# Performance work log

Hardware: AMD Instinct MI355X
Metric: run time of the kernel (lower is better)

The kernel has to match this reference:

```python
import jax, jax.numpy as jnp
import numpy as np

B, D, H, O, E = 8192, 1024, 4096, 1024, 3

def setup_inputs() -> dict:
    key = jax.random.key(0)
    ks = jax.random.split(key, 8)
    s = lambda fan_in: 1.0 / np.sqrt(fan_in)
    return {
        "x":   jax.random.normal(ks[0], (B, D), jnp.float32),
        "gw1": jax.random.normal(ks[1], (D, 256), jnp.float32) * s(D),
        "gb1": jnp.zeros((256,), jnp.float32),
        "gw2": jax.random.normal(ks[2], (256, 128), jnp.float32) * s(256),
        "gb2": jnp.zeros((128,), jnp.float32),
        "gw3": jax.random.normal(ks[3], (128, E), jnp.float32) * s(128),
        "gb3": jnp.zeros((E,), jnp.float32),
        "ew1": jax.random.normal(ks[4], (E, D, H), jnp.float32) * s(D),
        "eb1": jnp.zeros((E, H), jnp.float32),
        "ew2": jax.random.normal(ks[5], (E, H, O), jnp.float32) * s(H),
        "eb2": jnp.zeros((E, O), jnp.float32),
        "top_k": 2,
    }

def reference(x, gw1, gb1, gw2, gb2, gw3, gb3, ew1, eb1, ew2, eb2, top_k):
    # Gating network (dropout is identity in eval mode)
    g = jax.nn.relu(x @ gw1 + gb1)
    g = jax.nn.relu(g @ gw2 + gb2)
    gates = jax.nn.softmax(g @ gw3 + gb3, axis=-1)          # [B, E]

    # top-k routing with renormalized weights
    topk_scores, topk_idx = jax.lax.top_k(gates, top_k)     # [B, k]
    topk_scores = topk_scores / jnp.sum(topk_scores, axis=-1, keepdims=True)

    # scatter normalized scores into dense [B, E] combine weights
    b_ix = jnp.arange(x.shape[0])[:, None]
    combine = jnp.zeros_like(gates).at[b_ix, topk_idx].add(topk_scores)  # [B, E]

    # run all experts densely (small E=3), combine with routing weights
    eh = jax.nn.relu(jnp.einsum('bd,edh->beh', x, ew1) + eb1[None])      # [B, E, H]
    eo = jnp.einsum('beh,eho->beo', eh, ew2) + eb2[None]                 # [B, E, O]
    out = jnp.einsum('be,beo->bo', combine, eo)                          # [B, O]
    return out, gates
```

## Files before the change

### kernel.cpp

```cpp
#include <hip/hip_runtime.h>
#include <cstdint>
#include <cstddef>

#define B_ROWS 8192
#define D_DIM  1024
#define H_DIM  4096
#define O_DIM  1024
#define E_NUM  3
#define K2     (2 * H_DIM)
#define MT256  34
#define SLOT_MAX (MT256 * 256)

typedef __attribute__((ext_vector_type(4))) float f4;
typedef __attribute__((ext_vector_type(8))) _Float16 half8;

__device__ __forceinline__ unsigned short f2h_bits(float f) {
  _Float16 h = (_Float16)f;
  return __builtin_bit_cast(unsigned short, h);
}

__device__ __forceinline__ void async16(const void* g, void* l) {
  __builtin_amdgcn_global_load_lds(
      (const __attribute__((address_space(1))) unsigned int*)g,
      (__attribute__((address_space(3))) unsigned int*)l, 16, 0, 0);
}

__global__ __launch_bounds__(256) void k_cast_x(const float* __restrict__ in,
                                                unsigned short* __restrict__ out) {
  size_t i = (size_t)blockIdx.x * 256 + threadIdx.x;
  const f4* p = (const f4*)in;
  f4 a = p[2 * i], b = p[2 * i + 1];
  half8 h;
#pragma unroll
  for (int j = 0; j < 4; ++j) { h[j] = (_Float16)a[j]; h[4 + j] = (_Float16)b[j]; }
  *(half8*)(out + 8 * i) = h;
}

__global__ __launch_bounds__(256) void k_transpose_cast(const float* __restrict__ in,
                                                        unsigned short* __restrict__ out,
                                                        int R, int C) {
  __shared__ float tile[32][33];
  const size_t eoff = (size_t)blockIdx.z * R * C;
  const float* I = in + eoff;
  unsigned short* O = out + eoff;
  int c0 = blockIdx.x * 32, r0 = blockIdx.y * 32;
  int tx = threadIdx.x & 31, ty = threadIdx.x >> 5;
#pragma unroll
  for (int i = 0; i < 4; ++i)
    tile[ty + 8 * i][tx] = I[(size_t)(r0 + ty + 8 * i) * C + c0 + tx];
  __syncthreads();
#pragma unroll
  for (int i = 0; i < 4; ++i)
    O[(size_t)(c0 + ty + 8 * i) * R + r0 + tx] = f2h_bits(tile[tx][ty + 8 * i]);
}

__global__ __launch_bounds__(256) void k_gemm_f32(const float* __restrict__ A,
                                                  const float* __restrict__ Bm,
                                                  const float* __restrict__ bias,
                                                  float* __restrict__ C,
                                                  int N, int K) {
  __shared__ float sAT[16][68];
  __shared__ float sB[16][68];
  const int t = threadIdx.x;
  const int tx = t & 15, ty = t >> 4;
  const int m0 = blockIdx.y * 64, n0 = blockIdx.x * 64;
  float acc[4][4] = {};
  for (int k0 = 0; k0 < K; k0 += 16) {
    __syncthreads();
#pragma unroll
    for (int i = 0; i < 4; ++i) {
      int idx = t + i * 256;
      int r = idx >> 4, c = idx & 15;
      sAT[c][r] = A[(size_t)(m0 + r) * K + (k0 + c)];
      int rb = idx >> 6, cb = idx & 63;
      sB[rb][cb] = Bm[(size_t)(k0 + rb) * N + (n0 + cb)];
    }
    __syncthreads();
#pragma unroll
    for (int kk = 0; kk < 16; ++kk) {
      f4 av = *(const f4*)&sAT[kk][ty * 4];
      f4 bv = *(const f4*)&sB[kk][tx * 4];
#pragma unroll
      for (int i = 0; i < 4; ++i)
#pragma unroll
        for (int j = 0; j < 4; ++j)
          acc[i][j] = fmaf(av[i], bv[j], acc[i][j]);
    }
  }
#pragma unroll
  for (int i = 0; i < 4; ++i) {
    int row = m0 + ty * 4 + i;
    f4 v;
#pragma unroll
    for (int j = 0; j < 4; ++j)
      v[j] = fmaxf(acc[i][j] + bias[n0 + tx * 4 + j], 0.f);
    *(f4*)&C[(size_t)row * N + n0 + tx * 4] = v;
  }
}

__global__ __launch_bounds__(256) void k_gate_topk(const float* __restrict__ h2,
                                                   const float* __restrict__ gw3,
                                                   const float* __restrict__ gb3,
                                                   float* __restrict__ gates,
                                                   float* __restrict__ combine,
                                                   int* __restrict__ bucket) {
  const int lane = threadIdx.x & 63;
  const int row = blockIdx.x * 4 + (threadIdx.x >> 6);
  const float* h = h2 + (size_t)row * 128;
  float h0 = h[lane], h1 = h[lane + 64];
  float l0 = h0 * gw3[lane * 3 + 0] + h1 * gw3[(lane + 64) * 3 + 0];
  float l1 = h0 * gw3[lane * 3 + 1] + h1 * gw3[(lane + 64) * 3 + 1];
  float l2 = h0 * gw3[lane * 3 + 2] + h1 * gw3[(lane + 64) * 3 + 2];
#pragma unroll
  for (int off = 32; off > 0; off >>= 1) {
    l0 += __shfl_down(l0, off);
    l1 += __shfl_down(l1, off);
    l2 += __shfl_down(l2, off);
  }
  if (lane == 0) {
    float g0 = l0 + gb3[0], g1v = l1 + gb3[1], g2v = l2 + gb3[2];
    float mx = fmaxf(g0, fmaxf(g1v, g2v));
    float e0 = expf(g0 - mx), e1 = expf(g1v - mx), e2 = expf(g2v - mx);
    float inv = 1.f / (e0 + e1 + e2);
    float p0 = e0 * inv, p1 = e1 * inv, p2 = e2 * inv;
    gates[row * 3 + 0] = p0; gates[row * 3 + 1] = p1; gates[row * 3 + 2] = p2;
    int amin = 0; float pm = p0;
    if (p1 <= pm) { pm = p1; amin = 1; }
    if (p2 <= pm) { pm = p2; amin = 2; }
    float denom = (p0 + p1 + p2) - pm;
    combine[row * 3 + 0] = (amin == 0) ? 0.f : p0 / denom;
    combine[row * 3 + 1] = (amin == 1) ? 0.f : p1 / denom;
    combine[row * 3 + 2] = (amin == 2) ? 0.f : p2 / denom;
    bucket[row] = amin;
  }
}

__global__ __launch_bounds__(256) void k_count(const int* __restrict__ bucket,
                                               int* __restrict__ cnt) {
  int row = blockIdx.x * 256 + threadIdx.x;
  int b = bucket[row];
  int lane = threadIdx.x & 63;
#pragma unroll
  for (int bid = 0; bid < 3; ++bid) {
    unsigned long long m = __ballot(b == bid);
    if (m && b == bid) {
      int prefix = __popcll(m & ((1ull << lane) - 1));
      if (prefix == 0) atomicAdd(&cnt[bid], __popcll(m));
    }
  }
}

__global__ void k_meta(const int* __restrict__ cnt, int* __restrict__ meta,
                       int* __restrict__ cnt2) {
  int t0 = (cnt[0] + 255) >> 8;
  int t1 = (cnt[1] + 255) >> 8;
  int t2 = (cnt[2] + 255) >> 8;
  meta[0] = 0; meta[1] = t0; meta[2] = t0 + t1; meta[3] = t0 + t1 + t2;
  cnt2[0] = 0; cnt2[1] = 0; cnt2[2] = 0;
}

__global__ __launch_bounds__(256) void k_scatter(const int* __restrict__ bucket,
                                                 const int* __restrict__ meta,
                                                 int* __restrict__ cnt2,
                                                 int* __restrict__ sorted) {
  int row = blockIdx.x * 256 + threadIdx.x;
  int b = bucket[row];
  int lane = threadIdx.x & 63;
#pragma unroll
  for (int bid = 0; bid < 3; ++bid) {
    unsigned long long m = __ballot(b == bid);
    if (m) {
      int cntm = __popcll(m);
      int leader = __ffsll((unsigned long long)m) - 1;
      int base = 0;
      if (lane == leader) base = atomicAdd(&cnt2[bid], cntm);
      base = __shfl(base, leader);
      if (b == bid) {
        int prefix = __popcll(m & ((1ull << lane) - 1));
        sorted[meta[bid] * 256 + base + prefix] = row;
      }
    }
  }
}

__device__ __forceinline__ void bucket_experts(int b, int& ea, int& eb) {
  ea = (b == 0) ? 1 : 0;
  eb = (b == 2) ? 1 : 2;
}


#define BAR8()  do { __builtin_amdgcn_s_barrier(); __builtin_amdgcn_sched_barrier(0); } while (0)
#define LGKM0() do { asm volatile("s_waitcnt lgkmcnt(0)" ::: "memory"); __builtin_amdgcn_sched_barrier(0); } while (0)
#define VMW(n)  do { asm volatile("s_waitcnt vmcnt(" #n ")" ::: "memory"); __builtin_amdgcn_sched_barrier(0); } while (0)

#define STG_A(buf, h, kt) do { \
    async16(aptr[(h) * 2 + 0] + (size_t)(kt) * 64, smem + (buf) * 32768 + (h) * 16384 + t * 16); \
    async16(aptr[(h) * 2 + 1] + (size_t)(kt) * 64, smem + (buf) * 32768 + (h) * 16384 + 8192 + t * 16); \
  } while (0)
#define STG_B(buf, h, kt) do { \
    async16(bptr[(h) * 2 + 0] + (size_t)(kt) * 64, smem + 65536 + (buf) * 32768 + (h) * 16384 + t * 16); \
    async16(bptr[(h) * 2 + 1] + (size_t)(kt) * 64, smem + 65536 + (buf) * 32768 + (h) * 16384 + 8192 + t * 16); \
  } while (0)
#define LDA8(buf, mh) do { \
    _Pragma("unroll") \
    for (int mf = 0; mf < 4; ++mf) { \
      fa[mf][0] = *(const half8*)(smem + (buf) * 32768 + baseA + (mh) * 8192 + mf * 2048 + ck0); \
      fa[mf][1] = *(const half8*)(smem + (buf) * 32768 + baseA + (mh) * 8192 + mf * 2048 + ck1); \
    } } while (0)
#define LDB8(buf, nh) do { \
    _Pragma("unroll") \
    for (int nf2 = 0; nf2 < 2; ++nf2) { \
      fb[(nh) * 2 + nf2][0] = *(const half8*)(smem + (buf) * 32768 + baseB + ((nh) * 2 + nf2) * 2048 + ck0); \
      fb[(nh) * 2 + nf2][1] = *(const half8*)(smem + (buf) * 32768 + baseB + ((nh) * 2 + nf2) * 2048 + ck1); \
    } } while (0)
#define MM8(mh, nh) do { \
    _Pragma("unroll") \
    for (int mf = 0; mf < 4; ++mf) { \
      _Pragma("unroll") \
      for (int nf2 = 0; nf2 < 2; ++nf2) { \
        acc[(mh) * 4 + mf][(nh) * 2 + nf2] = __builtin_amdgcn_mfma_f32_16x16x32_f16( \
            fa[mf][0], fb[(nh) * 2 + nf2][0], acc[(mh) * 4 + mf][(nh) * 2 + nf2], 0, 0, 0); \
        acc[(mh) * 4 + mf][(nh) * 2 + nf2] = __builtin_amdgcn_mfma_f32_16x16x32_f16( \
            fa[mf][1], fb[(nh) * 2 + nf2][1], acc[(mh) * 4 + mf][(nh) * 2 + nf2], 0, 0, 0); \
      } } } while (0)

__global__ __launch_bounds__(512, 2) void k_expert_h8(const unsigned short* __restrict__ Xh,
                                                      const unsigned short* __restrict__ W1T,
                                                      const float* __restrict__ combine,
                                                      const float* __restrict__ eb1,
                                                      const int* __restrict__ sorted,
                                                      const int* __restrict__ meta,
                                                      unsigned short* __restrict__ EHS) {
  constexpr int K = D_DIM;
  const int mt = blockIdx.x;
  const int tb1 = meta[1], tb2 = meta[2], tb3 = meta[3];
  if (mt >= tb3) return;
  const int b = (mt >= tb2) ? 2 : (mt >= tb1) ? 1 : 0;
  int ea, ebx; bucket_experts(b, ea, ebx);
  const int z = blockIdx.z;
  const int e = z ? ebx : ea;
  const int slot0 = mt * 256;
  const int n0 = blockIdx.y * 256;

  __shared__ __align__(16) char smem[131072];
  __shared__ float sC[256];
  const int t = threadIdx.x;
  if (t < 256) {
    int r = sorted[slot0 + t];
    sC[t] = (r < 0) ? 0.f : combine[(size_t)r * 3 + e];
  }

  const int jrow = t >> 3;
  const int j = (t & 7) ^ (jrow & 7);
  const unsigned short* aptr[4];
  const unsigned short* bptr[4];
#pragma unroll
  for (int i = 0; i < 4; ++i) {
    int R = jrow + i * 64;
    int r = sorted[slot0 + R];
    int rr = (r < 0) ? 0 : r;
    aptr[i] = Xh + (size_t)rr * K + j * 8;
    bptr[i] = W1T + (size_t)e * H_DIM * K + (size_t)(n0 + R) * K + j * 8;
  }
  const int lane = t & 63;
  const int wid = t >> 6;
  const int wm = wid >> 2, wn = wid & 3;
  const int quad = lane >> 4, l16 = lane & 15;
  const int ck0 = ((quad) ^ (l16 & 7)) * 16;
  const int ck1 = ((4 + quad) ^ (l16 & 7)) * 16;
  const int baseA = (wm * 128 + l16) * 128;
  const int baseB = 65536 + (wn * 64 + l16) * 128;

  f4 acc[8][4] = {};
  half8 fa[4][2], fb[4][2];

  STG_A(0, 0, 0); STG_A(0, 1, 0); STG_B(0, 0, 0); STG_B(0, 1, 0);
  STG_B(1, 0, 1); STG_B(1, 1, 1);
  VMW(4); BAR8();

#pragma unroll 1
  for (int it = 0; it < 7; ++it) {
    const int kt = 2 * it;
    LDA8(0, 0); LDB8(0, 0); STG_A(1, 0, kt + 1);
    BAR8(); LGKM0();
    __builtin_amdgcn_s_setprio(1); MM8(0, 0); __builtin_amdgcn_s_setprio(0);
    BAR8();
    LDB8(0, 1); STG_A(1, 1, kt + 1);
    BAR8(); LGKM0();
    __builtin_amdgcn_s_setprio(1); MM8(0, 1); __builtin_amdgcn_s_setprio(0);
    BAR8();
    LDA8(0, 1); STG_B(0, 0, kt + 2);
    BAR8(); LGKM0();
    __builtin_amdgcn_s_setprio(1); MM8(1, 0); __builtin_amdgcn_s_setprio(0);
    BAR8();
    STG_A(0, 0, kt + 2);
    BAR8(); LGKM0();
    __builtin_amdgcn_s_setprio(1); MM8(1, 1); __builtin_amdgcn_s_setprio(0);
    VMW(4); BAR8();
    LDA8(1, 0); LDB8(1, 0); STG_A(0, 1, kt + 2);
    BAR8(); LGKM0();
    __builtin_amdgcn_s_setprio(1); MM8(0, 0); __builtin_amdgcn_s_setprio(0);
    BAR8();
    LDB8(1, 1); STG_B(0, 1, kt + 2);
    BAR8(); LGKM0();
    __builtin_amdgcn_s_setprio(1); MM8(0, 1); __builtin_amdgcn_s_setprio(0);
    BAR8();
    LDA8(1, 1); STG_B(1, 0, kt + 3);
    BAR8(); LGKM0();
    __builtin_amdgcn_s_setprio(1); MM8(1, 0); __builtin_amdgcn_s_setprio(0);
    BAR8();
    STG_B(1, 1, kt + 3);
    BAR8(); LGKM0();
    __builtin_amdgcn_s_setprio(1); MM8(1, 1); __builtin_amdgcn_s_setprio(0);
    VMW(4); BAR8();
  }
  {
    LDA8(0, 0); LDB8(0, 0); STG_A(1, 0, 15);
    BAR8(); LGKM0();
    __builtin_amdgcn_s_setprio(1); MM8(0, 0); __builtin_amdgcn_s_setprio(0);
    BAR8();
    LDB8(0, 1); STG_A(1, 1, 15);
    BAR8(); LGKM0();
    __builtin_amdgcn_s_setprio(1); MM8(0, 1); __builtin_amdgcn_s_setprio(0);
    BAR8();
    LDA8(0, 1);
    BAR8(); LGKM0();
    __builtin_amdgcn_s_setprio(1); MM8(1, 0); __builtin_amdgcn_s_setprio(0);
    BAR8();
    BAR8(); LGKM0();
    __builtin_amdgcn_s_setprio(1); MM8(1, 1); __builtin_amdgcn_s_setprio(0);
    VMW(0); BAR8();
    LDA8(1, 0); LDB8(1, 0); MM8(0, 0);
    LDB8(1, 1); MM8(0, 1);
    LDA8(1, 1); MM8(1, 0);
    MM8(1, 1);
  }

  const float* bias = eb1 + (size_t)e * H_DIM;
#pragma unroll
  for (int nf = 0; nf < 4; ++nf) {
    int col = n0 + wn * 64 + nf * 16 + l16;
    float bb = bias[col];
#pragma unroll
    for (int mf = 0; mf < 8; ++mf) {
#pragma unroll
      for (int r = 0; r < 4; ++r) {
        int rloc = wm * 128 + mf * 16 + quad * 4 + r;
        float v = fmaxf(acc[mf][nf][r] + bb, 0.f) * sC[rloc];
        EHS[(size_t)(slot0 + rloc) * K2 + (size_t)z * H_DIM + col] = f2h_bits(v);
      }
    }
  }
}

__global__ __launch_bounds__(256) void k_expert_o(const unsigned short* __restrict__ EHS,
                                                  const unsigned short* __restrict__ W2T,
                                                  const float* __restrict__ combine,
                                                  const float* __restrict__ eb2,
                                                  const int* __restrict__ sorted,
                                                  const int* __restrict__ meta,
                                                  float* __restrict__ OUT) {
  const int mt = blockIdx.x;
  const int tb1 = meta[1] * 2, tb2 = meta[2] * 2, tb3 = meta[3] * 2;
  if (mt >= tb3) return;
  const int b = (mt >= tb2) ? 2 : (mt >= tb1) ? 1 : 0;
  int ea, ebx; bucket_experts(b, ea, ebx);
  const int hz = blockIdx.z;
  const int e = hz ? ebx : ea;
  const int slot0 = mt * 128;
  const int n0 = blockIdx.y * 128;

  __shared__ __align__(16) char smem[32768];
  __shared__ int sRow[128];
  __shared__ float sCa[128], sCb[128];
  char* sA = smem;
  char* sB = smem + 16384;
  const int t = threadIdx.x;
  if (t < 128) {
    int r = sorted[slot0 + t];
    sRow[t] = r;
    int rr = (r < 0) ? 0 : r;
    sCa[t] = combine[(size_t)rr * 3 + ea];
    sCb[t] = combine[(size_t)rr * 3 + ebx];
  }

  const unsigned short* ap[4];
  size_t bpo[4];
  int soff[4];
#pragma unroll
  for (int i = 0; i < 4; ++i) {
    int sa = t + i * 256;
    int row = sa >> 3;
    int j = (sa & 7) ^ (row & 7);
    soff[i] = sa * 16;
    ap[i] = EHS + (size_t)(slot0 + row) * K2 + (size_t)hz * H_DIM + j * 8;
    bpo[i] = (size_t)(n0 + row) * H_DIM + j * 8;
  }
  const int lane = t & 63;
  const int wm = (t >> 6) & 1, wn = t >> 7;
  const int quad = lane >> 4, l16 = lane & 15;
  int offA[4][2], offB[4][2];
#pragma unroll
  for (int mtile = 0; mtile < 4; ++mtile) {
    int ra = wm * 64 + mtile * 16 + l16;
    int rb = wn * 64 + mtile * 16 + l16;
#pragma unroll
    for (int s = 0; s < 2; ++s) {
      offA[mtile][s] = ra * 128 + (((s * 4 + quad) ^ (ra & 7)) * 16);
      offB[mtile][s] = rb * 128 + (((s * 4 + quad) ^ (rb & 7)) * 16);
    }
  }
  f4 acc[4][4] = {};
  const unsigned short* Bb = W2T + (size_t)e * O_DIM * H_DIM;
  for (int k0 = 0; k0 < H_DIM; k0 += 64) {
#pragma unroll
    for (int i = 0; i < 4; ++i) {
      async16(ap[i] + k0, sA + soff[i]);
      async16(Bb + bpo[i] + k0, sB + soff[i]);
    }
    __syncthreads();
#pragma unroll
    for (int s = 0; s < 2; ++s) {
      half8 a[4], bfr[4];
#pragma unroll
      for (int i = 0; i < 4; ++i) a[i] = *(const half8*)(sA + offA[i][s]);
#pragma unroll
      for (int i = 0; i < 4; ++i) bfr[i] = *(const half8*)(sB + offB[i][s]);
#pragma unroll
      for (int i = 0; i < 4; ++i)
#pragma unroll
        for (int jn = 0; jn < 4; ++jn)
          acc[i][jn] = __builtin_amdgcn_mfma_f32_16x16x32_f16(a[i], bfr[jn], acc[i][jn], 0, 0, 0);
    }
    __syncthreads();
  }
#pragma unroll
  for (int nt = 0; nt < 4; ++nt) {
    int col = n0 + wn * 64 + nt * 16 + l16;
    float ba = eb2[(size_t)ea * O_DIM + col];
    float bb = eb2[(size_t)ebx * O_DIM + col];
#pragma unroll
    for (int mtile = 0; mtile < 4; ++mtile) {
#pragma unroll
      for (int r = 0; r < 4; ++r) {
        int rloc = wm * 64 + mtile * 16 + quad * 4 + r;
        int rowg = sRow[rloc];
        if (rowg >= 0) {
          float v = acc[mtile][nt][r];
          if (hz == 0) v += sCa[rloc] * ba + sCb[rloc] * bb;
          atomicAdd(&OUT[(size_t)rowg * O_DIM + col], v);
        }
      }
    }
  }
}

extern "C" void kernel_launch(void* const* d_in, const int* in_sizes, int n_in,
                              void* d_out, int out_size, void* d_ws, size_t ws_size,
                              hipStream_t stream) {
  const float* x   = (const float*)d_in[0];
  const float* gw1 = (const float*)d_in[1];
  const float* gb1 = (const float*)d_in[2];
  const float* gw2 = (const float*)d_in[3];
  const float* gb2 = (const float*)d_in[4];
  const float* gw3 = (const float*)d_in[5];
  const float* gb3 = (const float*)d_in[6];
  const float* ew1 = (const float*)d_in[7];
  const float* eb1 = (const float*)d_in[8];
  const float* ew2 = (const float*)d_in[9];
  const float* eb2 = (const float*)d_in[10];
  float* out = (float*)d_out;
  float* gates = out + (size_t)B_ROWS * O_DIM;

  char* ws = (char*)d_ws;
  size_t off = 0;
  auto take = [&](size_t bytes) -> char* {
    char* p = ws + off;
    off += (bytes + 255) & ~(size_t)255;
    return p;
  };
  unsigned short* xh  = (unsigned short*)take((size_t)B_ROWS * D_DIM * 2);
  unsigned short* w1t = (unsigned short*)take((size_t)E_NUM * H_DIM * D_DIM * 2);
  unsigned short* w2t = (unsigned short*)take((size_t)E_NUM * O_DIM * H_DIM * 2);
  float* comb   = (float*)take((size_t)B_ROWS * 3 * 4);
  float* g1     = (float*)take((size_t)B_ROWS * 256 * 4);
  float* h2     = (float*)take((size_t)B_ROWS * 128 * 4);
  int* bucket   = (int*)take((size_t)B_ROWS * 4);
  int* sorted   = (int*)take((size_t)SLOT_MAX * 4);
  int* cnt      = (int*)take(3 * 4);
  int* cnt2     = (int*)take(3 * 4);
  int* meta     = (int*)take(4 * 4);
  unsigned short* ehs = (unsigned short*)take((size_t)SLOT_MAX * K2 * 2);

  hipMemsetAsync(cnt, 0, 3 * 4, stream);
  hipMemsetAsync(sorted, 0xFF, (size_t)SLOT_MAX * 4, stream);
  hipMemsetAsync(out, 0, (size_t)B_ROWS * O_DIM * 4, stream);

  k_cast_x<<<dim3(B_ROWS * D_DIM / (256 * 8)), 256, 0, stream>>>(x, xh);
  k_transpose_cast<<<dim3(H_DIM / 32, D_DIM / 32, E_NUM), 256, 0, stream>>>(ew1, w1t, D_DIM, H_DIM);
  k_transpose_cast<<<dim3(O_DIM / 32, H_DIM / 32, E_NUM), 256, 0, stream>>>(ew2, w2t, H_DIM, O_DIM);

  k_gemm_f32<<<dim3(256 / 64, B_ROWS / 64), 256, 0, stream>>>(x, gw1, gb1, g1, 256, D_DIM);
  k_gemm_f32<<<dim3(128 / 64, B_ROWS / 64), 256, 0, stream>>>(g1, gw2, gb2, h2, 128, 256);
  k_gate_topk<<<dim3(B_ROWS / 4), 256, 0, stream>>>(h2, gw3, gb3, gates, comb, bucket);

  k_count<<<dim3(B_ROWS / 256), 256, 0, stream>>>(bucket, cnt);
  k_meta<<<1, 1, 0, stream>>>(cnt, meta, cnt2);
  k_scatter<<<dim3(B_ROWS / 256), 256, 0, stream>>>(bucket, meta, cnt2, sorted);

  k_expert_h8<<<dim3(MT256, H_DIM / 256, 2), 512, 0, stream>>>(
      xh, w1t, comb, eb1, sorted, meta, ehs);
  k_expert_o<<<dim3(MT256 * 2, O_DIM / 128, 2), 256, 0, stream>>>(
      ehs, w2t, comb, eb2, sorted, meta, out);
}
```

Baseline: 846.1 us.

## Port second expert GEMM to 256x256 pipelined 8-wave MFMA kernel

Factors the software-pipelined K loop of the first expert GEMM into a macro and reuses it for the second expert GEMM. The second GEMM moves from 128x128 tiles with 256 threads and a simple load-sync-compute loop to 256x256 tiles with 512 threads, double-buffered async LDS staging and interleaved MFMA phases. The aim is more data reuse per tile and better overlap of global loads with matrix math over the long K=4096 reduction. In exchange the grid has a quarter as many blocks, which can underfill the GPU, and each block needs a large LDS allocation and more registers. There is also a leftover unused per-row load of sorted indices.

```diff
diff --git a/kernel.cpp b/kernel.cpp
--- a/kernel.cpp
+++ b/kernel.cpp
@@ -224,6 +224,65 @@
             fa[mf][1], fb[(nh) * 2 + nf2][1], acc[(mh) * 4 + mf][(nh) * 2 + nf2], 0, 0, 0); \
       } } } while (0)
 
+#define KLOOP8(NITER, LASTKT) \
+  _Pragma("unroll 1") \
+  for (int it = 0; it < (NITER) - 1; ++it) { \
+    const int kt = 2 * it; \
+    LDA8(0, 0); LDB8(0, 0); STG_A(1, 0, kt + 1); \
+    BAR8(); LGKM0(); \
+    __builtin_amdgcn_s_setprio(1); MM8(0, 0); __builtin_amdgcn_s_setprio(0); \
+    BAR8(); \
+    LDB8(0, 1); STG_A(1, 1, kt + 1); \
+    BAR8(); LGKM0(); \
+    __builtin_amdgcn_s_setprio(1); MM8(0, 1); __builtin_amdgcn_s_setprio(0); \
+    BAR8(); \
+    LDA8(0, 1); STG_B(0, 0, kt + 2); \
+    BAR8(); LGKM0(); \
+    __builtin_amdgcn_s_setprio(1); MM8(1, 0); __builtin_amdgcn_s_setprio(0); \
+    BAR8(); \
+    STG_A(0, 0, kt + 2); \
+    BAR8(); LGKM0(); \
+    __builtin_amdgcn_s_setprio(1); MM8(1, 1); __builtin_amdgcn_s_setprio(0); \
+    VMW(4); BAR8(); \
+    LDA8(1, 0); LDB8(1, 0); STG_A(0, 1, kt + 2); \
+    BAR8(); LGKM0(); \
+    __builtin_amdgcn_s_setprio(1); MM8(0, 0); __builtin_amdgcn_s_setprio(0); \
+    BAR8(); \
+    LDB8(1, 1); STG_B(0, 1, kt + 2); \
+    BAR8(); LGKM0(); \
+    __builtin_amdgcn_s_setprio(1); MM8(0, 1); __builtin_amdgcn_s_setprio(0); \
+    BAR8(); \
+    LDA8(1, 1); STG_B(1, 0, kt + 3); \
+    BAR8(); LGKM0(); \
+    __builtin_amdgcn_s_setprio(1); MM8(1, 0); __builtin_amdgcn_s_setprio(0); \
+    BAR8(); \
+    STG_B(1, 1, kt + 3); \
+    BAR8(); LGKM0(); \
+    __builtin_amdgcn_s_setprio(1); MM8(1, 1); __builtin_amdgcn_s_setprio(0); \
+    VMW(4); BAR8(); \
+  } \
+  {  \
+    LDA8(0, 0); LDB8(0, 0); STG_A(1, 0, LASTKT); \
+    BAR8(); LGKM0(); \
+    __builtin_amdgcn_s_setprio(1); MM8(0, 0); __builtin_amdgcn_s_setprio(0); \
+    BAR8(); \
+    LDB8(0, 1); STG_A(1, 1, LASTKT); \
+    BAR8(); LGKM0(); \
+    __builtin_amdgcn_s_setprio(1); MM8(0, 1); __builtin_amdgcn_s_setprio(0); \
+    BAR8(); \
+    LDA8(0, 1); \
+    BAR8(); LGKM0(); \
+    __builtin_amdgcn_s_setprio(1); MM8(1, 0); __builtin_amdgcn_s_setprio(0); \
+    BAR8(); \
+    BAR8(); LGKM0(); \
+    __builtin_amdgcn_s_setprio(1); MM8(1, 1); __builtin_amdgcn_s_setprio(0); \
+    VMW(0); BAR8(); \
+    LDA8(1, 0); LDB8(1, 0); MM8(0, 0); \
+    LDB8(1, 1); MM8(0, 1); \
+    LDA8(1, 1); MM8(1, 0); \
+    MM8(1, 1); \
+  }
+
 __global__ __launch_bounds__(512, 2) void k_expert_h8(const unsigned short* __restrict__ Xh,
                                                       const unsigned short* __restrict__ W1T,
                                                       const float* __restrict__ combine,
@@ -278,63 +337,7 @@
   STG_B(1, 0, 1); STG_B(1, 1, 1);
   VMW(4); BAR8();
 
-#pragma unroll 1
-  for (int it = 0; it < 7; ++it) {
-    const int kt = 2 * it;
-    LDA8(0, 0); LDB8(0, 0); STG_A(1, 0, kt + 1);
-    BAR8(); LGKM0();
-    __builtin_amdgcn_s_setprio(1); MM8(0, 0); __builtin_amdgcn_s_setprio(0);
-    BAR8();
-    LDB8(0, 1); STG_A(1, 1, kt + 1);
-    BAR8(); LGKM0();
-    __builtin_amdgcn_s_setprio(1); MM8(0, 1); __builtin_amdgcn_s_setprio(0);
-    BAR8();
-    LDA8(0, 1); STG_B(0, 0, kt + 2);
-    BAR8(); LGKM0();
-    __builtin_amdgcn_s_setprio(1); MM8(1, 0); __builtin_amdgcn_s_setprio(0);
-    BAR8();
-    STG_A(0, 0, kt + 2);
-    BAR8(); LGKM0();
-    __builtin_amdgcn_s_setprio(1); MM8(1, 1); __builtin_amdgcn_s_setprio(0);
-    VMW(4); BAR8();
-    LDA8(1, 0); LDB8(1, 0); STG_A(0, 1, kt + 2);
-    BAR8(); LGKM0();
-    __builtin_amdgcn_s_setprio(1); MM8(0, 0); __builtin_amdgcn_s_setprio(0);
-    BAR8();
-    LDB8(1, 1); STG_B(0, 1, kt + 2);
-    BAR8(); LGKM0();
-    __builtin_amdgcn_s_setprio(1); MM8(0, 1); __builtin_amdgcn_s_setprio(0);
-    BAR8();
-    LDA8(1, 1); STG_B(1, 0, kt + 3);
-    BAR8(); LGKM0();
-    __builtin_amdgcn_s_setprio(1); MM8(1, 0); __builtin_amdgcn_s_setprio(0);
-    BAR8();
-    STG_B(1, 1, kt + 3);
-    BAR8(); LGKM0();
-    __builtin_amdgcn_s_setprio(1); MM8(1, 1); __builtin_amdgcn_s_setprio(0);
-    VMW(4); BAR8();
-  }
-  {
-    LDA8(0, 0); LDB8(0, 0); STG_A(1, 0, 15);
-    BAR8(); LGKM0();
-    __builtin_amdgcn_s_setprio(1); MM8(0, 0); __builtin_amdgcn_s_setprio(0);
-    BAR8();
-    LDB8(0, 1); STG_A(1, 1, 15);
-    BAR8(); LGKM0();
-    __builtin_amdgcn_s_setprio(1); MM8(0, 1); __builtin_amdgcn_s_setprio(0);
-    BAR8();
-    LDA8(0, 1);
-    BAR8(); LGKM0();
-    __builtin_amdgcn_s_setprio(1); MM8(1, 0); __builtin_amdgcn_s_setprio(0);
-    BAR8();
-    BAR8(); LGKM0();
-    __builtin_amdgcn_s_setprio(1); MM8(1, 1); __builtin_amdgcn_s_setprio(0);
-    VMW(0); BAR8();
-    LDA8(1, 0); LDB8(1, 0); MM8(0, 0);
-    LDB8(1, 1); MM8(0, 1);
-    LDA8(1, 1); MM8(1, 0);
-    MM8(1, 1);
-  }
+  KLOOP8(8, 15)
 
   const float* bias = eb1 + (size_t)e * H_DIM;
 #pragma unroll
@@ -353,30 +356,28 @@
   }
 }
 
-__global__ __launch_bounds__(256) void k_expert_o(const unsigned short* __restrict__ EHS,
-                                                  const unsigned short* __restrict__ W2T,
-                                                  const float* __restrict__ combine,
-                                                  const float* __restrict__ eb2,
-                                                  const int* __restrict__ sorted,
-                                                  const int* __restrict__ meta,
-                                                  float* __restrict__ OUT) {
+__global__ __launch_bounds__(512, 2) void k_expert_o8(const unsigned short* __restrict__ EHS,
+                                                      const unsigned short* __restrict__ W2T,
+                                                      const float* __restrict__ combine,
+                                                      const float* __restrict__ eb2,
+                                                      const int* __restrict__ sorted,
+                                                      const int* __restrict__ meta,
+                                                      float* __restrict__ OUT) {
   const int mt = blockIdx.x;
-  const int tb1 = meta[1] * 2, tb2 = meta[2] * 2, tb3 = meta[3] * 2;
+  const int tb1 = meta[1], tb2 = meta[2], tb3 = meta[3];
   if (mt >= tb3) return;
   const int b = (mt >= tb2) ? 2 : (mt >= tb1) ? 1 : 0;
   int ea, ebx; bucket_experts(b, ea, ebx);
   const int hz = blockIdx.z;
   const int e = hz ? ebx : ea;
-  const int slot0 = mt * 128;
-  const int n0 = blockIdx.y * 128;
-
-  __shared__ __align__(16) char smem[32768];
-  __shared__ int sRow[128];
-  __shared__ float sCa[128], sCb[128];
-  char* sA = smem;
-  char* sB = smem + 16384;
+  const int slot0 = mt * 256;
+  const int n0 = blockIdx.y * 256;
+
+  __shared__ __align__(16) char smem[131072];
+  __shared__ int sRow[256];
+  __shared__ float sCa[256], sCb[256];
   const int t = threadIdx.x;
-  if (t < 128) {
+  if (t < 256) {
     int r = sorted[slot0 + t];
     sRow[t] = r;
     int rr = (r < 0) ? 0 : r;
@@ -384,69 +385,50 @@
     sCb[t] = combine[(size_t)rr * 3 + ebx];
   }
 
-  const unsigned short* ap[4];
-  size_t bpo[4];
-  int soff[4];
+  const int jrow = t >> 3;
+  const int j = (t & 7) ^ (jrow & 7);
+  const unsigned short* aptr[4];
+  const unsigned short* bptr[4];
 #pragma unroll
   for (int i = 0; i < 4; ++i) {
-    int sa = t + i * 256;
-    int row = sa >> 3;
-    int j = (sa & 7) ^ (row & 7);
-    soff[i] = sa * 16;
-    ap[i] = EHS + (size_t)(slot0 + row) * K2 + (size_t)hz * H_DIM + j * 8;
-    bpo[i] = (size_t)(n0 + row) * H_DIM + j * 8;
+    int R = jrow + i * 64;
+    int r = sorted[slot0 + R];
+    int rr = (r < 0) ? 0 : r;
+    aptr[i] = EHS + (size_t)(slot0 + R) * K2 + (size_t)hz * H_DIM + j * 8;
+    (void)rr;
+    bptr[i] = W2T + (size_t)e * O_DIM * H_DIM + (size_t)(n0 + R) * H_DIM + j * 8;
   }
   const int lane = t & 63;
-  const int wm = (t >> 6) & 1, wn = t >> 7;
+  const int wid = t >> 6;
+  const int wm = wid >> 2, wn = wid & 3;
   const int quad = lane >> 4, l16 = lane & 15;
-  int offA[4][2], offB[4][2];
-#pragma unroll
-  for (int mtile = 0; mtile < 4; ++mtile) {
-    int ra = wm * 64 + mtile * 16 + l16;
-    int rb = wn * 64 + mtile * 16 + l16;
-#pragma unroll
-    for (int s = 0; s < 2; ++s) {
-      offA[mtile][s] = ra * 128 + (((s * 4 + quad) ^ (ra & 7)) * 16);
-      offB[mtile][s] = rb * 128 + (((s * 4 + quad) ^ (rb & 7)) * 16);
-    }
-  }
-  f4 acc[4][4] = {};
-  const unsigned short* Bb = W2T + (size_t)e * O_DIM * H_DIM;
-  for (int k0 = 0; k0 < H_DIM; k0 += 64) {
-#pragma unroll
-    for (int i = 0; i < 4; ++i) {
-      async16(ap[i] + k0, sA + soff[i]);
-      async16(Bb + bpo[i] + k0, sB + soff[i]);
-    }
-    __syncthreads();
-#pragma unroll
-    for (int s = 0; s < 2; ++s) {
-      half8 a[4], bfr[4];
-#pragma unroll
-      for (int i = 0; i < 4; ++i) a[i] = *(const half8*)(sA + offA[i][s]);
-#pragma unroll
-      for (int i = 0; i < 4; ++i) bfr[i] = *(const half8*)(sB + offB[i][s]);
-#pragma unroll
-      for (int i = 0; i < 4; ++i)
-#pragma unroll
-        for (int jn = 0; jn < 4; ++jn)
-          acc[i][jn] = __builtin_amdgcn_mfma_f32_16x16x32_f16(a[i], bfr[jn], acc[i][jn], 0, 0, 0);
-    }
-    __syncthreads();
-  }
-#pragma unroll
-  for (int nt = 0; nt < 4; ++nt) {
-    int col = n0 + wn * 64 + nt * 16 + l16;
+  const int ck0 = ((quad) ^ (l16 & 7)) * 16;
+  const int ck1 = ((4 + quad) ^ (l16 & 7)) * 16;
+  const int baseA = (wm * 128 + l16) * 128;
+  const int baseB = 65536 + (wn * 64 + l16) * 128;
+
+  f4 acc[8][4] = {};
+  half8 fa[4][2], fb[4][2];
+
+  STG_A(0, 0, 0); STG_A(0, 1, 0); STG_B(0, 0, 0); STG_B(0, 1, 0);
+  STG_B(1, 0, 1); STG_B(1, 1, 1);
+  VMW(4); BAR8();
+
+  KLOOP8(32, 63)
+
+#pragma unroll
+  for (int nf = 0; nf < 4; ++nf) {
+    int col = n0 + wn * 64 + nf * 16 + l16;
     float ba = eb2[(size_t)ea * O_DIM + col];
     float bb = eb2[(size_t)ebx * O_DIM + col];
 #pragma unroll
-    for (int mtile = 0; mtile < 4; ++mtile) {
+    for (int mf = 0; mf < 8; ++mf) {
 #pragma unroll
       for (int r = 0; r < 4; ++r) {
-        int rloc = wm * 64 + mtile * 16 + quad * 4 + r;
+        int rloc = wm * 128 + mf * 16 + quad * 4 + r;
         int rowg = sRow[rloc];
         if (rowg >= 0) {
-          float v = acc[mtile][nt][r];
+          float v = acc[mf][nf][r];
           if (hz == 0) v += sCa[rloc] * ba + sCb[rloc] * bb;
           atomicAdd(&OUT[(size_t)rowg * O_DIM + col], v);
         }
@@ -510,6 +492,6 @@
 
   k_expert_h8<<<dim3(MT256, H_DIM / 256, 2), 512, 0, stream>>>(
       xh, w1t, comb, eb1, sorted, meta, ehs);
-  k_expert_o<<<dim3(MT256 * 2, O_DIM / 128, 2), 256, 0, stream>>>(
+  k_expert_o8<<<dim3(MT256, O_DIM / 256, 2), 512, 0, stream>>>(
       ehs, w2t, comb, eb2, sorted, meta, out);
 }
```

After: 743.1 us. 12.2% less time.
